# Optimization experiments

Hardware: AMD Instinct MI355X
Metric: run time of the kernel (lower is better)

The kernel has to match this reference:

```python
import jax, jax.numpy as jnp
import numpy as np

N = 131072   # n_agents
K = 2        # k_neighbors = k_obstacles
H, C = 4, 128
HC = H * C   # 512
OBS_DIM = 37
OUT = 4


def setup_inputs() -> dict:
    key = jax.random.key(0)
    ks = jax.random.split(key, 40)
    s = 0.05
    def g(i, shape):
        return jax.random.normal(ks[i], shape, dtype=jnp.float32) * s
    inp = {"obs": jax.random.normal(ks[0], (N, OBS_DIM), dtype=jnp.float32)}
    # layer 0 (query_dim = 19)
    inp["wq0"] = g(1, (19, HC)); inp["wak0"] = g(2, (6, HC)); inp["wav0"] = g(3, (7, HC))
    inp["wok0"] = g(4, (2, HC)); inp["wov0"] = g(5, (2, HC))
    inp["apw0"] = g(6, (HC, C)); inp["apb0"] = jnp.zeros((C,), jnp.float32)
    inp["opw0"] = g(7, (HC, C)); inp["opb0"] = jnp.zeros((C,), jnp.float32)
    inp["fpw0"] = g(8, (2 * C, C)); inp["fpb0"] = jnp.zeros((C,), jnp.float32)
    inp["ca0"] = jnp.float32(1.0); inp["co0"] = jnp.float32(2.0)
    # layer 1 (query_dim = gnn_hidden_dim = 128)
    inp["wq1"] = g(9, (C, HC)); inp["wak1"] = g(10, (6, HC)); inp["wav1"] = g(11, (7, HC))
    inp["wok1"] = g(12, (2, HC)); inp["wov1"] = g(13, (2, HC))
    inp["apw1"] = g(14, (HC, C)); inp["apb1"] = jnp.zeros((C,), jnp.float32)
    inp["opw1"] = g(15, (HC, C)); inp["opb1"] = jnp.zeros((C,), jnp.float32)
    inp["fpw1"] = g(16, (2 * C, C)); inp["fpb1"] = jnp.zeros((C,), jnp.float32)
    inp["ca1"] = jnp.float32(1.0); inp["co1"] = jnp.float32(2.0)
    # output head
    inp["headw"] = g(17, (C, OUT)); inp["headb"] = jnp.zeros((OUT,), jnp.float32)
    return inp


def _forward(obs, wq0, wak0, wav0, wok0, wov0, apw0, apb0, opw0, opb0, fpw0, fpb0, ca0, co0,
             wq1, wak1, wav1, wok1, wov1, apw1, apb1, opw1, opb1, fpw1, fpb1, ca1, co1,
             headw, headb):
    n = obs.shape[0]
    scale = (C // H) ** -0.5  # matches torch: (out_channels // heads) ** -0.5

    # feature extraction per ObservationConfig (k=2)
    qf = jnp.concatenate([obs[:, 0:12], obs[:, 30:37]], axis=-1)        # [n, 19]
    nb = obs[:, 12:24].reshape(n, K, 6)                                  # neighbor keys [n,k,6]
    nbv = jnp.concatenate([nb, obs[:, 24:26][..., None]], axis=-1)       # + progress -> [n,k,7]
    ob = obs[:, 26:30].reshape(n, K, 2)                                  # obstacle k/v [n,k,2]
    apos = obs[:, 0:2]
    npos = nb[..., 0:2]
    opos = ob

    def attend(q, kfeat, vfeat, wk, wv, pw, pb, decay, pos_k):
        keys = (kfeat @ wk).reshape(n, K, H, C)
        vals = (vfeat @ wv).reshape(n, K, H, C)
        dist = jnp.linalg.norm(apos[:, None, :] - pos_k, axis=-1)        # [n,k]
        dw = jnp.exp(-decay * dist)                                      # [n,k]
        dot = jnp.einsum('nhc,nkhc->nhk', q, keys) * scale
        att = jax.nn.softmax(dot * dw[:, None, :], axis=-1)
        out = jnp.einsum('nhk,nkhc->nhc', att, vals).reshape(n, HC)
        return out @ pw + pb                                             # [n, C]

    def layer(qfeat, wq, wak, wav, wok, wov, apw, apb, opw, opb, fpw, fpb, ca, co):
        q = (qfeat @ wq).reshape(n, H, C)
        a = attend(q, nb, nbv, wak, wav, apw, apb, ca, npos)
        o = attend(q, ob, ob, wok, wov, opw, opb, co, opos)
        return jnp.concatenate([a, o], axis=-1) @ fpw + fpb              # [n, C]

    h = layer(qf, wq0, wak0, wav0, wok0, wov0, apw0, apb0, opw0, opb0, fpw0, fpb0, ca0, co0)
    h = layer(h, wq1, wak1, wav1, wok1, wov1, apw1, apb1, opw1, opb1, fpw1, fpb1, ca1, co1)
    return h @ headw + headb                                             # [n, OUT]


def reference(obs, wq0, wak0, wav0, wok0, wov0, apw0, apb0, opw0, opb0, fpw0, fpb0, ca0, co0,
              wq1, wak1, wav1, wok1, wov1, apw1, apb1, opw1, opb1, fpw1, fpb1, ca1, co1,
              headw, headb):
    return _forward(obs, wq0, wak0, wav0, wok0, wov0, apw0, apb0, opw0, opb0, fpw0, fpb0, ca0, co0,
                    wq1, wak1, wav1, wok1, wov1, apw1, apb1, opw1, opb1, fpw1, fpb1, ca1, co1,
                    headw, headb)
```

## Files before the change

### kernel.cpp

```cpp
#include <hip/hip_runtime.h>
#include <math.h>

#define NTH 256

enum : int {
  WQ0_OFF = 0,
  M_OFF   = 608,
  TB_OFF  = 1760,
  AO1_OFF = 1792,
  B1H_OFF = 1936,
  TBL_N   = 1940,
  WQ1_OFF = 1952,
  AO0_OFF = 6048,
  PA0_OFF = 10656,
  PO0_OFF = 14240,
  PA1_OFF = 15264,
  PO1_OFF = 18848,
  F1T_OFF = 19872,
  F1B_OFF = 20384,
  B0_OFF  = 20896,
  BB1_OFF = 21024,
  WS_END  = 21152
};

__global__ void prep1(
    const float* __restrict__ wq0, const float* __restrict__ wak0, const float* __restrict__ wok0,
    const float* __restrict__ wq1, const float* __restrict__ wak1, const float* __restrict__ wok1,
    const float* __restrict__ wav0, const float* __restrict__ apw0,
    const float* __restrict__ wov0, const float* __restrict__ opw0,
    const float* __restrict__ wav1, const float* __restrict__ apw1,
    const float* __restrict__ wov1, const float* __restrict__ opw1,
    const float* __restrict__ fpw1, const float* __restrict__ headw,
    const float* __restrict__ fpw0,
    const float* __restrict__ fpb0, const float* __restrict__ apb0, const float* __restrict__ opb0,
    const float* __restrict__ fpb1, const float* __restrict__ apb1, const float* __restrict__ opb1,
    float* __restrict__ ws)
{
  int gid = blockIdx.x * NTH + threadIdx.x;
  if (gid < 608) {
    int j = gid & 7, r = (gid >> 3) % 19, h = gid / 152;
    const float* a = wq0 + r * 512 + h * 128;
    const float* b = ((j < 6) ? (wak0 + j * 512) : (wok0 + (j - 6) * 512)) + h * 128;
    float acc = 0.f;
    for (int c = 0; c < 128; c++) acc += a[c] * b[c];
    ws[WQ0_OFF + gid] = acc;
  } else if (gid < 4704) {
    int idx = gid - 608;
    int j = idx & 7, cc = (idx >> 3) & 127, h = idx >> 10;
    const float* a = wq1 + cc * 512 + h * 128;
    const float* b = ((j < 6) ? (wak1 + j * 512) : (wok1 + (j - 6) * 512)) + h * 128;
    float acc = 0.f;
    for (int c = 0; c < 128; c++) acc += a[c] * b[c];
    ws[WQ1_OFF + idx] = acc;
  } else if (gid < 8288) {
    int idx = gid - 4704;
    int t = idx & 127, i = (idx >> 7) % 7, h = idx / 896;
    const float* w = wav0 + i * 512 + h * 128;
    const float* p = apw0 + (h * 128) * 128 + t;
    float acc = 0.f;
    for (int c = 0; c < 128; c++) acc += w[c] * p[c * 128];
    ws[PA0_OFF + idx] = acc;
  } else if (gid < 9312) {
    int idx = gid - 8288;
    int t = idx & 127, i = (idx >> 7) & 1, h = idx >> 8;
    const float* w = wov0 + i * 512 + h * 128;
    const float* p = opw0 + (h * 128) * 128 + t;
    float acc = 0.f;
    for (int c = 0; c < 128; c++) acc += w[c] * p[c * 128];
    ws[PO0_OFF + idx] = acc;
  } else if (gid < 12896) {
    int idx = gid - 9312;
    int t = idx & 127, i = (idx >> 7) % 7, h = idx / 896;
    const float* w = wav1 + i * 512 + h * 128;
    const float* p = apw1 + (h * 128) * 128 + t;
    float acc = 0.f;
    for (int c = 0; c < 128; c++) acc += w[c] * p[c * 128];
    ws[PA1_OFF + idx] = acc;
  } else if (gid < 13920) {
    int idx = gid - 12896;
    int t = idx & 127, i = (idx >> 7) & 1, h = idx >> 8;
    const float* w = wov1 + i * 512 + h * 128;
    const float* p = opw1 + (h * 128) * 128 + t;
    float acc = 0.f;
    for (int c = 0; c < 128; c++) acc += w[c] * p[c * 128];
    ws[PO1_OFF + idx] = acc;
  } else if (gid < 14432) {
    int idx = gid - 13920;
    int o2 = idx & 3, i = idx >> 2;
    float acc = 0.f;
    for (int j = 0; j < 128; j++) acc += fpw1[i * 128 + j] * headw[j * 4 + o2];
    ws[F1T_OFF + idx] = acc;
  } else if (gid < 14944) {
    int idx = gid - 14432;
    int o2 = idx & 3, i = idx >> 2;
    float acc = 0.f;
    for (int j = 0; j < 128; j++) acc += fpw1[(128 + i) * 128 + j] * headw[j * 4 + o2];
    ws[F1B_OFF + idx] = acc;
  } else if (gid < 15072) {
    int j = gid - 14944;
    float acc = fpb0[j];
    for (int c = 0; c < 128; c++)
      acc += apb0[c] * fpw0[c * 128 + j] + opb0[c] * fpw0[(128 + c) * 128 + j];
    ws[B0_OFF + j] = acc;
  } else if (gid < 15200) {
    int j = gid - 15072;
    float acc = fpb1[j];
    for (int c = 0; c < 128; c++)
      acc += apb1[c] * fpw1[c * 128 + j] + opb1[c] * fpw1[(128 + c) * 128 + j];
    ws[BB1_OFF + j] = acc;
  }
}

__global__ void prep2(
    const float* __restrict__ fpw0, const float* __restrict__ headw,
    const float* __restrict__ headb, float* __restrict__ ws)
{
  int gid = blockIdx.x * NTH + threadIdx.x;
  if (gid < 4608) {
    int j = gid & 127, i = (gid >> 7) % 9, h = gid / 1152;
    float acc = 0.f;
    if (i < 7) {
      const float* P = ws + PA0_OFF + (h * 7 + i) * 128;
      for (int u = 0; u < 128; u++) acc += P[u] * fpw0[u * 128 + j];
    } else {
      const float* P = ws + PO0_OFF + (h * 2 + (i - 7)) * 128;
      for (int u = 0; u < 128; u++) acc += P[u] * fpw0[(128 + u) * 128 + j];
    }
    ws[AO0_OFF + gid] = acc;
  } else if (gid < 4752) {
    int idx = gid - 4608;
    int o2 = idx & 3, i = (idx >> 2) % 9, h = idx / 36;
    float acc = 0.f;
    if (i < 7) {
      const float* P = ws + PA1_OFF + (h * 7 + i) * 128;
      for (int u = 0; u < 128; u++) acc += P[u] * ws[F1T_OFF + u * 4 + o2];
    } else {
      const float* P = ws + PO1_OFF + (h * 2 + (i - 7)) * 128;
      for (int u = 0; u < 128; u++) acc += P[u] * ws[F1B_OFF + u * 4 + o2];
    }
    ws[AO1_OFF + idx] = acc;
  } else if (gid < 4784) {
    int idx = gid - 4752;
    int j = idx & 7, h = idx >> 3;
    float acc = 0.f;
    for (int cc = 0; cc < 128; cc++)
      acc += ws[B0_OFF + cc] * ws[WQ1_OFF + h * 1024 + cc * 8 + j];
    ws[TB_OFF + idx] = acc;
  } else if (gid < 4788) {
    int o2 = gid - 4784;
    float acc = headb[o2];
    for (int j = 0; j < 128; j++) acc += ws[BB1_OFF + j] * headw[j * 4 + o2];
    ws[B1H_OFF + o2] = acc;
  }
}

__global__ void prep3(float* __restrict__ ws)
{
  int gid = blockIdx.x * NTH + threadIdx.x;
  if (gid < 1152) {
    int hj = gid & 31, t = gid >> 5;
    int h = hj >> 3, j = hj & 7;
    float acc = 0.f;
    const float* A = ws + AO0_OFF + t * 128;
    const float* W = ws + WQ1_OFF + h * 1024 + j;
    for (int c = 0; c < 128; c++) acc += A[c] * W[c * 8];
    ws[M_OFF + gid] = acc;
  }
}

__global__ __launch_bounds__(NTH) void actor_main(
    const float* __restrict__ obs, const float* __restrict__ ws,
    const float* __restrict__ pca0, const float* __restrict__ pco0,
    const float* __restrict__ pca1, const float* __restrict__ pco1,
    float* __restrict__ out, int n)
{
  __shared__ float4 stbl[485];
  __shared__ float sobs[NTH * 37];
  const int tid = threadIdx.x;
  const int m0 = blockIdx.x * NTH;
  int rows = n - m0; if (rows > NTH) rows = NTH;

  for (int i = tid; i < 485; i += NTH) stbl[i] = ((const float4*)ws)[i];
  {
    const float4* gsrc = (const float4*)(obs + (size_t)m0 * 37);
    float4* dst = (float4*)sobs;
    int tot = rows * 37, tot4 = tot >> 2;
    for (int i = tid; i < tot4; i += NTH) dst[i] = gsrc[i];
    if (tid < (tot & 3)) sobs[(tot4 << 2) + tid] = obs[(size_t)m0 * 37 + (tot4 << 2) + tid];
  }
  __syncthreads();
  if (tid >= rows) return;

  const float* o = sobs + tid * 37;
  const float scale = 0.17677669529663687f;

  float qf[19];
#pragma unroll
  for (int i = 0; i < 12; i++) qf[i] = o[i];
#pragma unroll
  for (int i = 0; i < 7; i++) qf[12 + i] = o[30 + i];
  float nb[2][6];
#pragma unroll
  for (int k2 = 0; k2 < 2; k2++)
#pragma unroll
    for (int i = 0; i < 6; i++) nb[k2][i] = o[12 + 6 * k2 + i];
  const float nbv6[2] = { o[24], o[25] };
  const float obf[2][2] = { { o[26], o[27] }, { o[28], o[29] } };
  const float ax = o[0], ay = o[1];

  float dista[2], disto[2];
#pragma unroll
  for (int k2 = 0; k2 < 2; k2++) {
    float dx = ax - nb[k2][0], dy = ay - nb[k2][1];
    dista[k2] = sqrtf(dx * dx + dy * dy);
    float ex = ax - obf[k2][0], ey = ay - obf[k2][1];
    disto[k2] = sqrtf(ex * ex + ey * ey);
  }
  const float ca0 = pca0[0], co0 = pco0[0], ca1 = pca1[0], co1 = pco1[0];
  float dwa0[2], dwo0[2], dwa1[2], dwo1[2];
#pragma unroll
  for (int k2 = 0; k2 < 2; k2++) {
    dwa0[k2] = __expf(-ca0 * dista[k2]);
    dwo0[k2] = __expf(-co0 * disto[k2]);
    dwa1[k2] = __expf(-ca1 * dista[k2]);
    dwo1[k2] = __expf(-co1 * disto[k2]);
  }

  float t0[32];
#pragma unroll
  for (int z = 0; z < 32; z++) t0[z] = 0.f;
#pragma unroll
  for (int h = 0; h < 4; h++) {
#pragma unroll
    for (int r = 0; r < 19; r++) {
      float q = qf[r];
      float4 w0 = stbl[(h * 19 + r) * 2 + 0];
      float4 w1 = stbl[(h * 19 + r) * 2 + 1];
      t0[h * 8 + 0] += q * w0.x; t0[h * 8 + 1] += q * w0.y;
      t0[h * 8 + 2] += q * w0.z; t0[h * 8 + 3] += q * w0.w;
      t0[h * 8 + 4] += q * w1.x; t0[h * 8 + 5] += q * w1.y;
      t0[h * 8 + 6] += q * w1.z; t0[h * 8 + 7] += q * w1.w;
    }
  }

  float wff[36];
#pragma unroll
  for (int h = 0; h < 4; h++) {
    float la[2], lo[2];
#pragma unroll
    for (int k2 = 0; k2 < 2; k2++) {
      float da = t0[h*8+0]*nb[k2][0] + t0[h*8+1]*nb[k2][1] + t0[h*8+2]*nb[k2][2]
               + t0[h*8+3]*nb[k2][3] + t0[h*8+4]*nb[k2][4] + t0[h*8+5]*nb[k2][5];
      la[k2] = da * scale * dwa0[k2];
      float dof = t0[h*8+6]*obf[k2][0] + t0[h*8+7]*obf[k2][1];
      lo[k2] = dof * scale * dwo0[k2];
    }
    float e  = __expf(la[1] - la[0]); float aa1 = e  / (1.f + e);  float aa0 = 1.f - aa1;
    float eo = __expf(lo[1] - lo[0]); float bo1 = eo / (1.f + eo); float bo0 = 1.f - bo1;
#pragma unroll
    for (int i = 0; i < 6; i++) wff[h * 9 + i] = aa0 * nb[0][i] + aa1 * nb[1][i];
    wff[h * 9 + 6] = aa0 * nbv6[0] + aa1 * nbv6[1];
    wff[h * 9 + 7] = bo0 * obf[0][0] + bo1 * obf[1][0];
    wff[h * 9 + 8] = bo0 * obf[0][1] + bo1 * obf[1][1];
  }

  float t1f[32];
#pragma unroll
  for (int q = 0; q < 8; q++) {
    float4 b = stbl[440 + q];
    t1f[4*q] = b.x; t1f[4*q+1] = b.y; t1f[4*q+2] = b.z; t1f[4*q+3] = b.w;
  }
#pragma unroll
  for (int t = 0; t < 36; t++) {
    float f = wff[t];
#pragma unroll
    for (int q = 0; q < 8; q++) {
      float4 m = stbl[152 + t * 8 + q];
      t1f[4*q]   += f * m.x; t1f[4*q+1] += f * m.y;
      t1f[4*q+2] += f * m.z; t1f[4*q+3] += f * m.w;
    }
  }

  float wf1f[36];
#pragma unroll
  for (int h = 0; h < 4; h++) {
    float la[2], lo[2];
#pragma unroll
    for (int k2 = 0; k2 < 2; k2++) {
      float da = t1f[h*8+0]*nb[k2][0] + t1f[h*8+1]*nb[k2][1] + t1f[h*8+2]*nb[k2][2]
               + t1f[h*8+3]*nb[k2][3] + t1f[h*8+4]*nb[k2][4] + t1f[h*8+5]*nb[k2][5];
      la[k2] = da * scale * dwa1[k2];
      float dof = t1f[h*8+6]*obf[k2][0] + t1f[h*8+7]*obf[k2][1];
      lo[k2] = dof * scale * dwo1[k2];
    }
    float e  = __expf(la[1] - la[0]); float aa1 = e  / (1.f + e);  float aa0 = 1.f - aa1;
    float eo = __expf(lo[1] - lo[0]); float bo1 = eo / (1.f + eo); float bo0 = 1.f - bo1;
#pragma unroll
    for (int i = 0; i < 6; i++) wf1f[h * 9 + i] = aa0 * nb[0][i] + aa1 * nb[1][i];
    wf1f[h * 9 + 6] = aa0 * nbv6[0] + aa1 * nbv6[1];
    wf1f[h * 9 + 7] = bo0 * obf[0][0] + bo1 * obf[1][0];
    wf1f[h * 9 + 8] = bo0 * obf[0][1] + bo1 * obf[1][1];
  }

  float4 acc = stbl[484];
#pragma unroll
  for (int t = 0; t < 36; t++) {
    float f = wf1f[t];
    float4 w = stbl[448 + t];
    acc.x += f * w.x; acc.y += f * w.y; acc.z += f * w.z; acc.w += f * w.w;
  }
  ((float4*)out)[m0 + tid] = acc;
}

extern "C" void kernel_launch(void* const* d_in, const int* in_sizes, int n_in,
                              void* d_out, int out_size, void* d_ws, size_t ws_size,
                              hipStream_t stream)
{
  const float* obs  = (const float*)d_in[0];
  const float* wq0  = (const float*)d_in[1];
  const float* wak0 = (const float*)d_in[2];
  const float* wav0 = (const float*)d_in[3];
  const float* wok0 = (const float*)d_in[4];
  const float* wov0 = (const float*)d_in[5];
  const float* apw0 = (const float*)d_in[6];
  const float* apb0 = (const float*)d_in[7];
  const float* opw0 = (const float*)d_in[8];
  const float* opb0 = (const float*)d_in[9];
  const float* fpw0 = (const float*)d_in[10];
  const float* fpb0 = (const float*)d_in[11];
  const float* ca0  = (const float*)d_in[12];
  const float* co0  = (const float*)d_in[13];
  const float* wq1  = (const float*)d_in[14];
  const float* wak1 = (const float*)d_in[15];
  const float* wav1 = (const float*)d_in[16];
  const float* wok1 = (const float*)d_in[17];
  const float* wov1 = (const float*)d_in[18];
  const float* apw1 = (const float*)d_in[19];
  const float* apb1 = (const float*)d_in[20];
  const float* opw1 = (const float*)d_in[21];
  const float* opb1 = (const float*)d_in[22];
  const float* fpw1 = (const float*)d_in[23];
  const float* fpb1 = (const float*)d_in[24];
  const float* ca1  = (const float*)d_in[25];
  const float* co1  = (const float*)d_in[26];
  const float* headw = (const float*)d_in[27];
  const float* headb = (const float*)d_in[28];
  float* ws = (float*)d_ws;
  int n = in_sizes[0] / 37;

  prep1<<<(15200 + NTH - 1) / NTH, NTH, 0, stream>>>(
      wq0, wak0, wok0, wq1, wak1, wok1,
      wav0, apw0, wov0, opw0, wav1, apw1, wov1, opw1,
      fpw1, headw, fpw0, fpb0, apb0, opb0, fpb1, apb1, opb1, ws);
  prep2<<<(4788 + NTH - 1) / NTH, NTH, 0, stream>>>(fpw0, headw, headb, ws);
  prep3<<<(1152 + NTH - 1) / NTH, NTH, 0, stream>>>(ws);
  actor_main<<<(n + NTH - 1) / NTH, NTH, 0, stream>>>(
      obs, ws, ca0, co0, ca1, co1, (float*)d_out, n);
}
```

Before: 175.2 us.

## Merge prep2/prep3 into one block kernel and load obs directly per thread

Fuses the second and third weight-precompute kernels into a single 1024-thread block that keeps intermediate AO0 and WQ1 in shared memory, removing one launch and a global round-trip. The main kernel drops its shared-memory staging of observation rows and has each thread read its 37 floats straight from global memory. That frees about 37KB of LDS per block, which should raise occupancy, but the per-thread strided loads are less coalesced. The merged prep now runs on only one block, which serialises its work onto a single CU.

```diff
diff --git a/kernel.cpp b/kernel.cpp
--- a/kernel.cpp
+++ b/kernel.cpp
@@ -11,16 +11,15 @@
   B1H_OFF = 1936,
   TBL_N   = 1940,
   WQ1_OFF = 1952,
-  AO0_OFF = 6048,
-  PA0_OFF = 10656,
-  PO0_OFF = 14240,
-  PA1_OFF = 15264,
-  PO1_OFF = 18848,
-  F1T_OFF = 19872,
-  F1B_OFF = 20384,
-  B0_OFF  = 20896,
-  BB1_OFF = 21024,
-  WS_END  = 21152
+  PA0_OFF = 6048,
+  PO0_OFF = 9632,
+  PA1_OFF = 10656,
+  PO1_OFF = 14240,
+  F1T_OFF = 15264,
+  F1B_OFF = 15776,
+  B0_OFF  = 16288,
+  BB1_OFF = 16416,
+  WS_END  = 16544
 };
 
 __global__ void prep1(
@@ -111,60 +110,69 @@
   }
 }
 
-__global__ void prep2(
+__global__ __launch_bounds__(1024) void prep23(
     const float* __restrict__ fpw0, const float* __restrict__ headw,
     const float* __restrict__ headb, float* __restrict__ ws)
 {
-  int gid = blockIdx.x * NTH + threadIdx.x;
-  if (gid < 4608) {
-    int j = gid & 127, i = (gid >> 7) % 9, h = gid / 1152;
-    float acc = 0.f;
-    if (i < 7) {
-      const float* P = ws + PA0_OFF + (h * 7 + i) * 128;
-      for (int u = 0; u < 128; u++) acc += P[u] * fpw0[u * 128 + j];
+  __shared__ float sAO0[4608];
+  __shared__ float sWQ1[4128];
+  __shared__ float sF[1024];
+  const int tid = threadIdx.x;
+
+  for (int g = tid; g < 4096; g += 1024)
+    sWQ1[(g >> 10) * 1032 + (g & 1023)] = ws[WQ1_OFF + g];
+  for (int g = tid; g < 1024; g += 1024)
+    sF[g] = ws[F1T_OFF + g];
+  __syncthreads();
+
+  for (int g = tid; g < 4788; g += 1024) {
+    if (g < 4608) {
+      int j = g & 127, i = (g >> 7) % 9, h = g / 1152;
+      float acc = 0.f;
+      if (i < 7) {
+        const float* P = ws + PA0_OFF + (h * 7 + i) * 128;
+        for (int u = 0; u < 128; u++) acc += P[u] * fpw0[u * 128 + j];
+      } else {
+        const float* P = ws + PO0_OFF + (h * 2 + (i - 7)) * 128;
+        for (int u = 0; u < 128; u++) acc += P[u] * fpw0[(128 + u) * 128 + j];
+      }
+      sAO0[g] = acc;
+    } else if (g < 4752) {
+      int idx = g - 4608;
+      int o2 = idx & 3, i = (idx >> 2) % 9, h = idx / 36;
+      float acc = 0.f;
+      if (i < 7) {
+        const float* P = ws + PA1_OFF + (h * 7 + i) * 128;
+        for (int u = 0; u < 128; u++) acc += P[u] * sF[u * 4 + o2];
+      } else {
+        const float* P = ws + PO1_OFF + (h * 2 + (i - 7)) * 128;
+        for (int u = 0; u < 128; u++) acc += P[u] * sF[512 + u * 4 + o2];
+      }
+      ws[AO1_OFF + idx] = acc;
+    } else if (g < 4784) {
+      int idx = g - 4752;
+      int j = idx & 7, h = idx >> 3;
+      float acc = 0.f;
+      for (int cc = 0; cc < 128; cc++)
+        acc += ws[B0_OFF + cc] * sWQ1[h * 1032 + cc * 8 + j];
+      ws[TB_OFF + idx] = acc;
     } else {
-      const float* P = ws + PO0_OFF + (h * 2 + (i - 7)) * 128;
-      for (int u = 0; u < 128; u++) acc += P[u] * fpw0[(128 + u) * 128 + j];
-    }
-    ws[AO0_OFF + gid] = acc;
-  } else if (gid < 4752) {
-    int idx = gid - 4608;
-    int o2 = idx & 3, i = (idx >> 2) % 9, h = idx / 36;
-    float acc = 0.f;
-    if (i < 7) {
-      const float* P = ws + PA1_OFF + (h * 7 + i) * 128;
-      for (int u = 0; u < 128; u++) acc += P[u] * ws[F1T_OFF + u * 4 + o2];
-    } else {
-      const float* P = ws + PO1_OFF + (h * 2 + (i - 7)) * 128;
-      for (int u = 0; u < 128; u++) acc += P[u] * ws[F1B_OFF + u * 4 + o2];
-    }
-    ws[AO1_OFF + idx] = acc;
-  } else if (gid < 4784) {
-    int idx = gid - 4752;
-    int j = idx & 7, h = idx >> 3;
-    float acc = 0.f;
-    for (int cc = 0; cc < 128; cc++)
-      acc += ws[B0_OFF + cc] * ws[WQ1_OFF + h * 1024 + cc * 8 + j];
-    ws[TB_OFF + idx] = acc;
-  } else if (gid < 4788) {
-    int o2 = gid - 4784;
-    float acc = headb[o2];
-    for (int j = 0; j < 128; j++) acc += ws[BB1_OFF + j] * headw[j * 4 + o2];
-    ws[B1H_OFF + o2] = acc;
-  }
-}
-
-__global__ void prep3(float* __restrict__ ws)
-{
-  int gid = blockIdx.x * NTH + threadIdx.x;
-  if (gid < 1152) {
-    int hj = gid & 31, t = gid >> 5;
+      int o2 = g - 4784;
+      float acc = headb[o2];
+      for (int j = 0; j < 128; j++) acc += ws[BB1_OFF + j] * headw[j * 4 + o2];
+      ws[B1H_OFF + o2] = acc;
+    }
+  }
+  __syncthreads();
+
+  for (int g = tid; g < 1152; g += 1024) {
+    int hj = g & 31, t = g >> 5;
     int h = hj >> 3, j = hj & 7;
     float acc = 0.f;
-    const float* A = ws + AO0_OFF + t * 128;
-    const float* W = ws + WQ1_OFF + h * 1024 + j;
+    const float* A = sAO0 + t * 128;
+    const float* W = sWQ1 + h * 1032 + j;
     for (int c = 0; c < 128; c++) acc += A[c] * W[c * 8];
-    ws[M_OFF + gid] = acc;
+    ws[M_OFF + g] = acc;
   }
 }
 
@@ -175,23 +183,19 @@
     float* __restrict__ out, int n)
 {
   __shared__ float4 stbl[485];
-  __shared__ float sobs[NTH * 37];
   const int tid = threadIdx.x;
-  const int m0 = blockIdx.x * NTH;
-  int rows = n - m0; if (rows > NTH) rows = NTH;
+  const int gid = blockIdx.x * NTH + tid;
 
   for (int i = tid; i < 485; i += NTH) stbl[i] = ((const float4*)ws)[i];
+  __syncthreads();
+  if (gid >= n) return;
+
+  float o[37];
   {
-    const float4* gsrc = (const float4*)(obs + (size_t)m0 * 37);
-    float4* dst = (float4*)sobs;
-    int tot = rows * 37, tot4 = tot >> 2;
-    for (int i = tid; i < tot4; i += NTH) dst[i] = gsrc[i];
-    if (tid < (tot & 3)) sobs[(tot4 << 2) + tid] = obs[(size_t)m0 * 37 + (tot4 << 2) + tid];
-  }
-  __syncthreads();
-  if (tid >= rows) return;
-
-  const float* o = sobs + tid * 37;
+    const float* op = obs + (size_t)gid * 37;
+#pragma unroll
+    for (int i = 0; i < 37; i++) o[i] = op[i];
+  }
   const float scale = 0.17677669529663687f;
 
   float qf[19];
@@ -309,7 +313,7 @@
     float4 w = stbl[448 + t];
     acc.x += f * w.x; acc.y += f * w.y; acc.z += f * w.z; acc.w += f * w.w;
   }
-  ((float4*)out)[m0 + tid] = acc;
+  ((float4*)out)[gid] = acc;
 }
 
 extern "C" void kernel_launch(void* const* d_in, const int* in_sizes, int n_in,
@@ -352,8 +356,7 @@
       wq0, wak0, wok0, wq1, wak1, wok1,
       wav0, apw0, wov0, opw0, wav1, apw1, wov1, opw1,
       fpw1, headw, fpw0, fpb0, apb0, opb0, fpb1, apb1, opb1, ws);
-  prep2<<<(4788 + NTH - 1) / NTH, NTH, 0, stream>>>(fpw0, headw, headb, ws);
-  prep3<<<(1152 + NTH - 1) / NTH, NTH, 0, stream>>>(ws);
+  prep23<<<1, 1024, 0, stream>>>(fpw0, headw, headb, ws);
   actor_main<<<(n + NTH - 1) / NTH, NTH, 0, stream>>>(
       obs, ws, ca0, co0, ca1, co1, (float*)d_out, n);
 }
```

New measurement: 208.0 us. +18.7%, slower.
